# Optimization experiments

Measured on AMD Instinct MI355X. Metric: run time of the kernel, lower is better.

## Reference

```python
import jax, jax.numpy as jnp
import numpy as np

B, N, DIM = 4, 2048, 1024
HEADS, DIM_HEAD = 16, 64
HIDDEN = HEADS * DIM_HEAD  # 1024
SCALE = 1.0 / np.sqrt(DIM_HEAD).astype(np.float32)


def setup_inputs() -> dict:
    key = jax.random.key(0)
    k1, k2, k3 = jax.random.split(key, 3)
    x = jax.random.normal(k1, (B, N, DIM), dtype=jnp.float32)
    # Linear(dim, 3*hidden, bias=False): stored as [in, out] for x @ W
    w_qkv = jax.random.normal(k2, (DIM, 3 * HIDDEN), dtype=jnp.float32) * (1.0 / np.sqrt(DIM))
    w_out = jax.random.normal(k3, (HIDDEN, DIM), dtype=jnp.float32) * (1.0 / np.sqrt(HIDDEN))
    b_out = jnp.zeros((DIM,), dtype=jnp.float32)
    return {"x": x, "w_qkv": w_qkv, "w_out": w_out, "b_out": b_out}


def reference(x, w_qkv, w_out, b_out):
    b, n, _ = x.shape
    qkv = x @ w_qkv                                  # [b, n, 3*hidden]
    q, k, v = jnp.split(qkv, 3, axis=-1)             # each [b, n, hidden]

    def to_heads(t):
        return t.reshape(b, n, HEADS, DIM_HEAD).transpose(0, 2, 1, 3)  # [b, h, n, d]

    q, k, v = to_heads(q), to_heads(k), to_heads(v)
    scores = jnp.einsum('bhid,bhjd->bhij', q, k) * SCALE   # [b, h, n_q, n_k]
    # Faithful to original: softmax over dim=2 (the QUERY axis), not keys.
    attn = jax.nn.softmax(scores, axis=2)
    y = jnp.einsum('bhij,bhjd->bhid', attn, v)             # [b, h, n, d]
    y = y.transpose(0, 2, 1, 3).reshape(b, n, HIDDEN)      # [b, n, hidden]
    return y @ w_out + b_out
```

## Files before the change

kernel.cpp:

```cpp
#include <hip/hip_runtime.h>
#include <math.h>
#include <stdint.h>

#define B_    4
#define N_    2048
#define DIM_  1024
#define H_    16
#define DH_   64
#define HID_  1024
#define RS_   3072
#define C2_   0.1803368801111204f

typedef unsigned short u16;
typedef unsigned int   u32;
typedef short  bf16x8 __attribute__((ext_vector_type(8)));
typedef u16    u16x8  __attribute__((ext_vector_type(8)));
typedef float  f32x4  __attribute__((ext_vector_type(4)));
typedef float  f32x16 __attribute__((ext_vector_type(16)));

__device__ inline u16 f2b(float x) {
    u32 u = __float_as_uint(x);
    return (u16)((u + 0x7fffu + ((u >> 16) & 1u)) >> 16);
}
__device__ inline float b2f(u16 x) {
    return __uint_as_float((u32)x << 16);
}

__device__ inline u32 pack2bf(float f0, float f1) {
    u32 u0 = __float_as_uint(f0) + 0x8000u;
    u32 u1 = __float_as_uint(f1) + 0x8000u;
    return __builtin_amdgcn_perm(u1, u0, 0x07060302u);
}

#if defined(__has_builtin)
#if __has_builtin(__builtin_amdgcn_global_load_lds)
#define USE_GLL 1
#endif
#endif

#ifdef USE_GLL
typedef const __attribute__((address_space(1))) u32* gas_ptr;
typedef __attribute__((address_space(3))) u32* las_ptr;
__device__ inline void gll16(const void* g, void* l) {
    __builtin_amdgcn_global_load_lds((gas_ptr)g, (las_ptr)l, 16, 0, 0);
}
#endif

__global__ __launch_bounds__(256) void cast_bf16(const float* __restrict__ in,
                                                 u16* __restrict__ out, int n) {
    int i = (blockIdx.x * 256 + threadIdx.x) * 8;
    if (i >= n) return;
    float4 a = *(const float4*)&in[i];
    float4 b = *(const float4*)&in[i + 4];
    u16x8 p;
    p[0] = f2b(a.x); p[1] = f2b(a.y); p[2] = f2b(a.z); p[3] = f2b(a.w);
    p[4] = f2b(b.x); p[5] = f2b(b.y); p[6] = f2b(b.z); p[7] = f2b(b.w);
    *(u16x8*)&out[i] = p;
}

__global__ __launch_bounds__(256) void transpose_cast(const float* __restrict__ W,
                                                      u16* __restrict__ Wt,
                                                      int K, int Nn, int qcols) {
    __shared__ float t[64][65];
    const int tid = threadIdx.x;
    const int k0 = blockIdx.y * 64, n0 = blockIdx.x * 64;
    for (int idx = tid; idx < 64 * 16; idx += 256) {
        int r = idx >> 4, c4 = (idx & 15) * 4;
        float4 g = *(const float4*)&W[(size_t)(k0 + r) * Nn + n0 + c4];
        t[r][c4] = g.x; t[r][c4 + 1] = g.y; t[r][c4 + 2] = g.z; t[r][c4 + 3] = g.w;
    }
    __syncthreads();
    for (int idx = tid; idx < 64 * 8; idx += 256) {
        int n = idx >> 3, k8 = (idx & 7) * 8;
        float s = (n0 + n < qcols) ? C2_ : 1.0f;
        u16x8 p;
        #pragma unroll
        for (int u = 0; u < 8; u++) p[u] = f2b(t[k8 + u][n] * s);
        *(u16x8*)&Wt[(size_t)(n0 + n) * K + k0 + k8] = p;
    }
}

template<int BF16OUT>
__global__ __launch_bounds__(256) void gemm_bt(const u16* __restrict__ A,
                                               const u16* __restrict__ Bt,
                                               const float* __restrict__ bias,
                                               void* __restrict__ Cout,
                                               int M, int Nn, int K) {
    __shared__ u16 at[128 * 32];
    __shared__ u16 bt[128 * 32];
    const int tid = threadIdx.x;
    const int lane = tid & 63, wave = tid >> 6;
    const int wr = wave >> 1, wc = wave & 1;
    const int mlane = lane & 15, quad = lane >> 4;
    const int id = blockIdx.x;
    const int mt = (id & 7) * 8 + ((id >> 3) & 7);
    const int nt = id >> 6;
    const int m0 = mt * 128, n0 = nt * 128;
    const int r = tid >> 2, kc = (tid & 3) * 8;

    f32x4 acc[4][4] = {};

    for (int k0 = 0; k0 < K; k0 += 32) {
        __syncthreads();
#ifdef USE_GLL
        gll16(&A[(size_t)(m0 + r) * K + k0 + kc],       &at[r * 32 + kc]);
        gll16(&A[(size_t)(m0 + r + 64) * K + k0 + kc],  &at[(r + 64) * 32 + kc]);
        gll16(&Bt[(size_t)(n0 + r) * K + k0 + kc],      &bt[r * 32 + kc]);
        gll16(&Bt[(size_t)(n0 + r + 64) * K + k0 + kc], &bt[(r + 64) * 32 + kc]);
#else
        *(u16x8*)&at[r * 32 + kc]        = *(const u16x8*)&A[(size_t)(m0 + r) * K + k0 + kc];
        *(u16x8*)&at[(r + 64) * 32 + kc] = *(const u16x8*)&A[(size_t)(m0 + r + 64) * K + k0 + kc];
        *(u16x8*)&bt[r * 32 + kc]        = *(const u16x8*)&Bt[(size_t)(n0 + r) * K + k0 + kc];
        *(u16x8*)&bt[(r + 64) * 32 + kc] = *(const u16x8*)&Bt[(size_t)(n0 + r + 64) * K + k0 + kc];
#endif
        __syncthreads();

        bf16x8 af[4], bf[4];
        #pragma unroll
        for (int rt = 0; rt < 4; rt++)
            af[rt] = *(const bf16x8*)&at[(wr * 64 + rt * 16 + mlane) * 32 + quad * 8];
        #pragma unroll
        for (int ct = 0; ct < 4; ct++)
            bf[ct] = *(const bf16x8*)&bt[(wc * 64 + ct * 16 + mlane) * 32 + quad * 8];
        #pragma unroll
        for (int rt = 0; rt < 4; rt++)
            #pragma unroll
            for (int ct = 0; ct < 4; ct++)
                acc[rt][ct] = __builtin_amdgcn_mfma_f32_16x16x32_bf16(af[rt], bf[ct], acc[rt][ct], 0, 0, 0);
    }

    const int row0 = m0 + wr * 64 + quad * 4;
    const int col0 = n0 + wc * 64 + mlane;
    #pragma unroll
    for (int rt = 0; rt < 4; rt++)
        #pragma unroll
        for (int ct = 0; ct < 4; ct++) {
            int c = col0 + ct * 16;
            float bv = (!BF16OUT && bias != nullptr) ? bias[c] : 0.f;
            #pragma unroll
            for (int reg = 0; reg < 4; reg++) {
                int rr = row0 + rt * 16 + reg;
                float v = acc[rt][ct][reg] + bv;
                if (BF16OUT) ((u16*)Cout)[(size_t)rr * Nn + c] = f2b(v);
                else         ((float*)Cout)[(size_t)rr * Nn + c] = v;
            }
        }
}

__global__ __launch_bounds__(256) void attn_stats_vt(const u16* __restrict__ qkvb,
                                                     u16* __restrict__ vT) {
    __shared__ u16 kt[64 * 72];
    __shared__ u16 qt[4][64 * 72];
    __shared__ float red[4][64];
    __shared__ float li[64];

    const int tid = threadIdx.x;
    const int lane = tid & 63, wave = tid >> 6;
    const int mlane = lane & 15, quad = lane >> 4;
    const int id = blockIdx.x;
    const int bh = (id & 7) * 8 + ((id >> 3) & 7);
    const int b = bh >> 4, h = bh & 15;
    const int j0 = (id >> 6) * 64;

    const u16* qbase = qkvb + (size_t)b * N_ * RS_ + h * DH_;
    const u16* kbase = qbase + HID_;
    const u16* vbase = qbase + 2 * HID_;

    for (int idx = tid; idx < 512; idx += 256) {
        int r = idx >> 3, d8 = (idx & 7) * 8;
        *(u16x8*)&kt[r * 72 + d8] = *(const u16x8*)&kbase[(size_t)(j0 + r) * RS_ + d8];
    }
    __syncthreads();

    bf16x8 kf[4][2];
    #pragma unroll
    for (int t = 0; t < 4; t++)
        #pragma unroll
        for (int ks = 0; ks < 2; ks++)
            kf[t][ks] = *(const bf16x8*)&kt[(t * 16 + mlane) * 72 + ks * 32 + quad * 8];

    f32x4 acc[4] = {};
    u16* qw = &qt[wave][0];

    const int prr = lane >> 3, pd8 = (lane & 7) * 8;
    u16x8 pq[8];
    #pragma unroll
    for (int t = 0; t < 8; t++)
        pq[t] = *(const u16x8*)&qbase[(size_t)(wave * 64 + t * 8 + prr) * RS_ + pd8];

    for (int i0 = wave * 64; i0 < N_; i0 += 256) {
        #pragma unroll
        for (int t = 0; t < 8; t++)
            *(u16x8*)&qw[(t * 8 + prr) * 72 + pd8] = pq[t];
        int in = i0 + 256;
        if (in < N_) {
            #pragma unroll
            for (int t = 0; t < 8; t++)
                pq[t] = *(const u16x8*)&qbase[(size_t)(in + t * 8 + prr) * RS_ + pd8];
        }
        #pragma unroll
        for (int q4 = 0; q4 < 4; q4++) {
            bf16x8 bq0 = *(const bf16x8*)&qw[(q4 * 16 + mlane) * 72 + quad * 8];
            bf16x8 bq1 = *(const bf16x8*)&qw[(q4 * 16 + mlane) * 72 + 32 + quad * 8];
            #pragma unroll
            for (int t = 0; t < 4; t++) {
                f32x4 z = {0.f, 0.f, 0.f, 0.f};
                z = __builtin_amdgcn_mfma_f32_16x16x32_bf16(kf[t][0], bq0, z, 0, 0, 0);
                z = __builtin_amdgcn_mfma_f32_16x16x32_bf16(kf[t][1], bq1, z, 0, 0, 0);
                #pragma unroll
                for (int reg = 0; reg < 4; reg++)
                    acc[t][reg] += __builtin_amdgcn_exp2f(z[reg]);
            }
        }
    }

    #pragma unroll
    for (int t = 0; t < 4; t++)
        #pragma unroll
        for (int reg = 0; reg < 4; reg++) {
            float v = acc[t][reg];
            v += __shfl_xor(v, 1, 64);
            v += __shfl_xor(v, 2, 64);
            v += __shfl_xor(v, 4, 64);
            v += __shfl_xor(v, 8, 64);
            if (mlane == 0) red[wave][t * 16 + quad * 4 + reg] = v;
        }
    __syncthreads();
    if (tid < 64) {
        float l = red[0][tid] + red[1][tid] + red[2][tid] + red[3][tid];
        li[tid] = 1.0f / l;
    }

    for (int idx = tid; idx < 512; idx += 256) {
        int r = idx >> 3, d8 = (idx & 7) * 8;
        *(u16x8*)&kt[r * 72 + d8] = *(const u16x8*)&vbase[(size_t)(j0 + r) * RS_ + d8];
    }
    __syncthreads();
    {
        int d = tid >> 2, j16 = (tid & 3) * 16;
        u16x8 p0, p1;
        #pragma unroll
        for (int u = 0; u < 8; u++) {
            p0[u] = f2b(b2f(kt[(j16 + u) * 72 + d]) * li[j16 + u]);
            p1[u] = f2b(b2f(kt[(j16 + 8 + u) * 72 + d]) * li[j16 + 8 + u]);
        }
        size_t o = ((size_t)bh * DH_ + d) * N_ + j0 + j16;
        *(u16x8*)&vT[o] = p0;
        *(u16x8*)&vT[o + 8] = p1;
    }
}

__global__ __launch_bounds__(256) void attn_apply(const u16* __restrict__ qkvb,
                                                  const u16* __restrict__ vT,
                                                  u16* __restrict__ yb) {
    __shared__ u16 S[256 * 72];

    const int tid = threadIdx.x;
    const int lane = tid & 63, wave = tid >> 6;
    const int m31 = lane & 31, half = lane >> 5;
    const int bh = blockIdx.y, b = bh >> 4, h = bh & 15;
    const int i0 = blockIdx.x * 256;

    const u16* qbase = qkvb + (size_t)b * N_ * RS_ + h * DH_;
    const u16* kbase = qbase + HID_;
    const u16* vbase = vT + (size_t)bh * DH_ * N_;

    for (int idx = tid; idx < 2048; idx += 256) {
        int r = idx >> 3, d8 = (idx & 7) * 8;
        *(u16x8*)&S[r * 72 + d8] = *(const u16x8*)&qbase[(size_t)(i0 + r) * RS_ + d8];
    }
    __syncthreads();

    bf16x8 qf[2][4];
    #pragma unroll
    for (int qc = 0; qc < 2; qc++)
        #pragma unroll
        for (int ks = 0; ks < 4; ks++)
            qf[qc][ks] = *(const bf16x8*)&S[(wave * 64 + qc * 32 + m31) * 72 + ks * 16 + half * 8];

    const int pr = tid >> 3, pc8 = (tid & 7) * 8;
    u16x8 pk0, pk1, pv0, pv1;
    pk0 = *(const u16x8*)&kbase[(size_t)pr * RS_ + pc8];
    pk1 = *(const u16x8*)&kbase[(size_t)(pr + 32) * RS_ + pc8];
    pv0 = *(const u16x8*)&vbase[(size_t)pr * N_ + pc8];
    pv1 = *(const u16x8*)&vbase[(size_t)(pr + 32) * N_ + pc8];

    f32x16 yacc[2][2] = {};

    for (int j0 = 0; j0 < N_; j0 += 64) {
        __syncthreads();
        *(u16x8*)&S[pr * 72 + pc8]        = pk0;
        *(u16x8*)&S[(pr + 32) * 72 + pc8] = pk1;
        *(u16x8*)&S[(pr + 64) * 72 + pc8] = pv0;
        *(u16x8*)&S[(pr + 96) * 72 + pc8] = pv1;
        __syncthreads();

        int jn = j0 + 64;
        if (jn < N_) {
            pk0 = *(const u16x8*)&kbase[(size_t)(jn + pr) * RS_ + pc8];
            pk1 = *(const u16x8*)&kbase[(size_t)(jn + pr + 32) * RS_ + pc8];
            pv0 = *(const u16x8*)&vbase[(size_t)pr * N_ + jn + pc8];
            pv1 = *(const u16x8*)&vbase[(size_t)(pr + 32) * N_ + jn + pc8];
        }

        bf16x8 pa[2][4];
        #pragma unroll
        for (int kt = 0; kt < 2; kt++) {
            bf16x8 ka[4];
            #pragma unroll
            for (int ks = 0; ks < 4; ks++)
                ka[ks] = *(const bf16x8*)&S[(kt * 32 + m31) * 72 + ks * 16 + half * 8];

            f32x16 sc[2] = {};
            #pragma unroll
            for (int ks = 0; ks < 4; ks++)
                #pragma unroll
                for (int qc = 0; qc < 2; qc++)
                    sc[qc] = __builtin_amdgcn_mfma_f32_32x32x16_bf16(ka[ks], qf[qc][ks], sc[qc], 0, 0, 0);

            #pragma unroll
            for (int qc = 0; qc < 2; qc++) {
                u32 U[4][2];
                #pragma unroll
                for (int rb = 0; rb < 4; rb++)
                    #pragma unroll
                    for (int pp = 0; pp < 2; pp++) {
                        float e0 = __builtin_amdgcn_exp2f(sc[qc][4 * rb + 2 * pp]);
                        float e1 = __builtin_amdgcn_exp2f(sc[qc][4 * rb + 2 * pp + 1]);
                        U[rb][pp] = pack2bf(e0, e1);
                    }
                #pragma unroll
                for (int ksl = 0; ksl < 2; ksl++) {
                    const int rb0 = 2 * ksl;
                    u32 a0 = U[rb0][0], a1 = U[rb0][1];
                    u32 b0 = U[rb0 + 1][0], b1 = U[rb0 + 1][1];
                    u32 e0 = half ? a0 : b0, e1 = half ? a1 : b1;
                    u32 g0 = (u32)__shfl_xor((int)e0, 32, 64);
                    u32 g1 = (u32)__shfl_xor((int)e1, 32, 64);
                    u32 o0 = half ? b0 : a0, o1 = half ? b1 : a1;
                    union { u32 u[4]; bf16x8 v; } cv;
                    cv.u[0] = half ? g0 : o0;
                    cv.u[1] = half ? g1 : o1;
                    cv.u[2] = half ? o0 : g0;
                    cv.u[3] = half ? o1 : g1;
                    pa[qc][2 * kt + ksl] = cv.v;
                }
            }
        }

        #pragma unroll
        for (int ks16 = 0; ks16 < 4; ks16++) {
            bf16x8 vb0 = *(const bf16x8*)&S[(64 + m31) * 72 + ks16 * 16 + half * 8];
            bf16x8 vb1 = *(const bf16x8*)&S[(96 + m31) * 72 + ks16 * 16 + half * 8];
            #pragma unroll
            for (int qc = 0; qc < 2; qc++) {
                yacc[qc][0] = __builtin_amdgcn_mfma_f32_32x32x16_bf16(pa[qc][ks16], vb0, yacc[qc][0], 0, 0, 0);
                yacc[qc][1] = __builtin_amdgcn_mfma_f32_32x32x16_bf16(pa[qc][ks16], vb1, yacc[qc][1], 0, 0, 0);
            }
        }
    }

    #pragma unroll
    for (int qc = 0; qc < 2; qc++)
        #pragma unroll
        for (int dt = 0; dt < 2; dt++)
            #pragma unroll
            for (int reg = 0; reg < 16; reg++) {
                int q = i0 + wave * 64 + qc * 32 + (reg & 3) + 8 * (reg >> 2) + 4 * half;
                yb[((size_t)b * N_ + q) * HID_ + h * DH_ + dt * 32 + m31] = f2b(yacc[qc][dt][reg]);
            }
}

extern "C" void kernel_launch(void* const* d_in, const int* in_sizes, int n_in,
                              void* d_out, int out_size, void* d_ws, size_t ws_size,
                              hipStream_t stream) {
    (void)in_sizes; (void)n_in; (void)out_size; (void)ws_size;

    const float* x     = (const float*)d_in[0];
    const float* w_qkv = (const float*)d_in[1];
    const float* w_out = (const float*)d_in[2];
    const float* b_out = (const float*)d_in[3];

    u16* xb    = (u16*)d_ws;
    u16* wqkvT = xb    + (size_t)8192 * 1024;
    u16* woutT = wqkvT + (size_t)3072 * 1024;
    u16* qkvb  = woutT + (size_t)1024 * 1024;
    u16* vTb   = qkvb  + (size_t)8192 * 3072;
    u16* yb    = vTb   + (size_t)64 * 64 * 2048;

    cast_bf16<<<4096, 256, 0, stream>>>(x, xb, 8192 * 1024);
    transpose_cast<<<dim3(3072 / 64, 1024 / 64), 256, 0, stream>>>(w_qkv, wqkvT, 1024, 3072, HID_);
    transpose_cast<<<dim3(1024 / 64, 1024 / 64), 256, 0, stream>>>(w_out, woutT, 1024, 1024, 0);

    gemm_bt<1><<<64 * 24, 256, 0, stream>>>(
        xb, wqkvT, nullptr, qkvb, 8192, 3072, 1024);

    attn_stats_vt<<<32 * 64, 256, 0, stream>>>(qkvb, vTb);

    attn_apply<<<dim3(N_ / 256, 64), 256, 0, stream>>>(qkvb, vTb, yb);

    gemm_bt<0><<<64 * 8, 256, 0, stream>>>(
        yb, woutT, b_out, d_out, 8192, 1024, 1024);
}
```

Measured before the change: 350.4 us.

## Split attention apply over key halves and sum partials in output GEMM

```diff
diff --git a/kernel.cpp b/kernel.cpp
--- a/kernel.cpp
+++ b/kernel.cpp
@@ -80,8 +80,9 @@
     }
 }
 
-template<int BF16OUT>
+template<int BF16OUT, int SUM2>
 __global__ __launch_bounds__(256) void gemm_bt(const u16* __restrict__ A,
+                                               const u16* __restrict__ A2,
                                                const u16* __restrict__ Bt,
                                                const float* __restrict__ bias,
                                                void* __restrict__ Cout,
@@ -102,17 +103,39 @@
 
     for (int k0 = 0; k0 < K; k0 += 32) {
         __syncthreads();
+        if (SUM2) {
+            size_t o0 = (size_t)(m0 + r) * K + k0 + kc;
+            size_t o1 = (size_t)(m0 + r + 64) * K + k0 + kc;
+            u16x8 a0 = *(const u16x8*)&A[o0],  c0 = *(const u16x8*)&A2[o0];
+            u16x8 a1 = *(const u16x8*)&A[o1],  c1 = *(const u16x8*)&A2[o1];
+            u16x8 s0, s1;
+            #pragma unroll
+            for (int u = 0; u < 8; u++) {
+                s0[u] = f2b(b2f((u16)a0[u]) + b2f((u16)c0[u]));
+                s1[u] = f2b(b2f((u16)a1[u]) + b2f((u16)c1[u]));
+            }
+            *(u16x8*)&at[r * 32 + kc]        = s0;
+            *(u16x8*)&at[(r + 64) * 32 + kc] = s1;
 #ifdef USE_GLL
-        gll16(&A[(size_t)(m0 + r) * K + k0 + kc],       &at[r * 32 + kc]);
-        gll16(&A[(size_t)(m0 + r + 64) * K + k0 + kc],  &at[(r + 64) * 32 + kc]);
-        gll16(&Bt[(size_t)(n0 + r) * K + k0 + kc],      &bt[r * 32 + kc]);
-        gll16(&Bt[(size_t)(n0 + r + 64) * K + k0 + kc], &bt[(r + 64) * 32 + kc]);
+            gll16(&Bt[(size_t)(n0 + r) * K + k0 + kc],      &bt[r * 32 + kc]);
+            gll16(&Bt[(size_t)(n0 + r + 64) * K + k0 + kc], &bt[(r + 64) * 32 + kc]);
 #else
-        *(u16x8*)&at[r * 32 + kc]        = *(const u16x8*)&A[(size_t)(m0 + r) * K + k0 + kc];
-        *(u16x8*)&at[(r + 64) * 32 + kc] = *(const u16x8*)&A[(size_t)(m0 + r + 64) * K + k0 + kc];
-        *(u16x8*)&bt[r * 32 + kc]        = *(const u16x8*)&Bt[(size_t)(n0 + r) * K + k0 + kc];
-        *(u16x8*)&bt[(r + 64) * 32 + kc] = *(const u16x8*)&Bt[(size_t)(n0 + r + 64) * K + k0 + kc];
+            *(u16x8*)&bt[r * 32 + kc]        = *(const u16x8*)&Bt[(size_t)(n0 + r) * K + k0 + kc];
+            *(u16x8*)&bt[(r + 64) * 32 + kc] = *(const u16x8*)&Bt[(size_t)(n0 + r + 64) * K + k0 + kc];
 #endif
+        } else {
+#ifdef USE_GLL
+            gll16(&A[(size_t)(m0 + r) * K + k0 + kc],       &at[r * 32 + kc]);
+            gll16(&A[(size_t)(m0 + r + 64) * K + k0 + kc],  &at[(r + 64) * 32 + kc]);
+            gll16(&Bt[(size_t)(n0 + r) * K + k0 + kc],      &bt[r * 32 + kc]);
+            gll16(&Bt[(size_t)(n0 + r + 64) * K + k0 + kc], &bt[(r + 64) * 32 + kc]);
+#else
+            *(u16x8*)&at[r * 32 + kc]        = *(const u16x8*)&A[(size_t)(m0 + r) * K + k0 + kc];
+            *(u16x8*)&at[(r + 64) * 32 + kc] = *(const u16x8*)&A[(size_t)(m0 + r + 64) * K + k0 + kc];
+            *(u16x8*)&bt[r * 32 + kc]        = *(const u16x8*)&Bt[(size_t)(n0 + r) * K + k0 + kc];
+            *(u16x8*)&bt[(r + 64) * 32 + kc] = *(const u16x8*)&Bt[(size_t)(n0 + r + 64) * K + k0 + kc];
+#endif
+        }
         __syncthreads();
 
         bf16x8 af[4], bf[4];
@@ -260,10 +283,13 @@
     const int m31 = lane & 31, half = lane >> 5;
     const int bh = blockIdx.y, b = bh >> 4, h = bh & 15;
     const int i0 = blockIdx.x * 256;
+    const int z = blockIdx.z;
+    const int jbase = z * (N_ / 2);
 
     const u16* qbase = qkvb + (size_t)b * N_ * RS_ + h * DH_;
     const u16* kbase = qbase + HID_;
     const u16* vbase = vT + (size_t)bh * DH_ * N_;
+    u16* ybz = yb + (size_t)z * (B_ * N_) * HID_;
 
     for (int idx = tid; idx < 2048; idx += 256) {
         int r = idx >> 3, d8 = (idx & 7) * 8;
@@ -280,14 +306,14 @@
 
     const int pr = tid >> 3, pc8 = (tid & 7) * 8;
     u16x8 pk0, pk1, pv0, pv1;
-    pk0 = *(const u16x8*)&kbase[(size_t)pr * RS_ + pc8];
-    pk1 = *(const u16x8*)&kbase[(size_t)(pr + 32) * RS_ + pc8];
-    pv0 = *(const u16x8*)&vbase[(size_t)pr * N_ + pc8];
-    pv1 = *(const u16x8*)&vbase[(size_t)(pr + 32) * N_ + pc8];
+    pk0 = *(const u16x8*)&kbase[(size_t)(jbase + pr) * RS_ + pc8];
+    pk1 = *(const u16x8*)&kbase[(size_t)(jbase + pr + 32) * RS_ + pc8];
+    pv0 = *(const u16x8*)&vbase[(size_t)pr * N_ + jbase + pc8];
+    pv1 = *(const u16x8*)&vbase[(size_t)(pr + 32) * N_ + jbase + pc8];
 
     f32x16 yacc[2][2] = {};
 
-    for (int j0 = 0; j0 < N_; j0 += 64) {
+    for (int j0 = jbase; j0 < jbase + N_ / 2; j0 += 64) {
         __syncthreads();
         *(u16x8*)&S[pr * 72 + pc8]        = pk0;
         *(u16x8*)&S[(pr + 32) * 72 + pc8] = pk1;
@@ -296,7 +322,7 @@
         __syncthreads();
 
         int jn = j0 + 64;
-        if (jn < N_) {
+        if (jn < jbase + N_ / 2) {
             pk0 = *(const u16x8*)&kbase[(size_t)(jn + pr) * RS_ + pc8];
             pk1 = *(const u16x8*)&kbase[(size_t)(jn + pr + 32) * RS_ + pc8];
             pv0 = *(const u16x8*)&vbase[(size_t)pr * N_ + jn + pc8];
@@ -367,7 +393,7 @@
             #pragma unroll
             for (int reg = 0; reg < 16; reg++) {
                 int q = i0 + wave * 64 + qc * 32 + (reg & 3) + 8 * (reg >> 2) + 4 * half;
-                yb[((size_t)b * N_ + q) * HID_ + h * DH_ + dt * 32 + m31] = f2b(yacc[qc][dt][reg]);
+                ybz[((size_t)b * N_ + q) * HID_ + h * DH_ + dt * 32 + m31] = f2b(yacc[qc][dt][reg]);
             }
 }
 
@@ -392,13 +418,13 @@
     transpose_cast<<<dim3(3072 / 64, 1024 / 64), 256, 0, stream>>>(w_qkv, wqkvT, 1024, 3072, HID_);
     transpose_cast<<<dim3(1024 / 64, 1024 / 64), 256, 0, stream>>>(w_out, woutT, 1024, 1024, 0);
 
-    gemm_bt<1><<<64 * 24, 256, 0, stream>>>(
-        xb, wqkvT, nullptr, qkvb, 8192, 3072, 1024);
+    gemm_bt<1, 0><<<64 * 24, 256, 0, stream>>>(
+        xb, nullptr, wqkvT, nullptr, qkvb, 8192, 3072, 1024);
 
     attn_stats_vt<<<32 * 64, 256, 0, stream>>>(qkvb, vTb);
 
-    attn_apply<<<dim3(N_ / 256, 64), 256, 0, stream>>>(qkvb, vTb, yb);
-
-    gemm_bt<0><<<64 * 8, 256, 0, stream>>>(
-        yb, woutT, b_out, d_out, 8192, 1024, 1024);
-}
+    attn_apply<<<dim3(N_ / 256, 64, 2), 256, 0, stream>>>(qkvb, vTb, yb);
+
+    gemm_bt<0, 1><<<64 * 8, 256, 0, stream>>>(
+        yb, yb + (size_t)8192 * 1024, woutT, b_out, d_out, 8192, 1024, 1024);
+}
```

Result: no change. 356.0 us (+1.6%).
